# Kernel tuning notes

Hardware: AMD Instinct MI355X
Metric: run time of the kernel (lower is better)

## Reference

```python
import jax, jax.numpy as jnp
import numpy as np

DIM = 512
HEADS = 8
DIM_HEAD = 64
INNER = HEADS * DIM_HEAD  # 512
HIDDEN = 512 * 4          # mlp_dim * expansion
EPS = 1e-5
SCALE = DIM_HEAD ** -0.5


def layernorm(x, w, b):
    mu = jnp.mean(x, axis=-1, keepdims=True)
    var = jnp.var(x, axis=-1, keepdims=True)
    return (x - mu) * jax.lax.rsqrt(var + EPS) * w + b


def setup_inputs() -> dict:
    key = jax.random.key(0)
    ks = jax.random.split(key, 12)
    B, P, N = 2, 8, 1024  # P must equal HEADS (axis-swap bug in original rearrange)
    s = lambda k, shape, fan: jax.random.normal(k, shape, jnp.float32) * (fan ** -0.5)
    return {
        "x": jax.random.normal(ks[0], (B, P, N, DIM), jnp.float32),
        "ln0_w": jnp.ones((DIM,), jnp.float32),
        "ln0_b": jnp.zeros((DIM,), jnp.float32),
        "ln1_w": jnp.ones((DIM,), jnp.float32),
        "ln1_b": jnp.zeros((DIM,), jnp.float32),
        "w_qkv": s(ks[1], (DIM, 3 * INNER), DIM),
        "w_o": s(ks[2], (INNER, DIM), INNER),
        "b_o": jnp.zeros((DIM,), jnp.float32),
        "w1": s(ks[3], (DIM, HIDDEN), DIM),
        "b1": jnp.zeros((HIDDEN,), jnp.float32),
        "w2": s(ks[4], (HIDDEN, DIM), HIDDEN),
        "b2": jnp.zeros((DIM,), jnp.float32),
    }


def reference(x, ln0_w, ln0_b, ln1_w, ln1_b, w_qkv, w_o, b_o, w1, b1, w2, b2):
    B, P, N, _ = x.shape
    x = layernorm(x, ln0_w, ln0_b)  # outer block norm

    # ---- VisionAttention ----
    h = layernorm(x, ln1_w, ln1_b)
    qkv = h @ w_qkv                                    # [B,P,N,3*INNER]
    q, k, v = jnp.split(qkv, 3, axis=-1)
    def to_heads(t):  # [B,P,N,H*D] -> [B,H,P,N,D]
        return t.reshape(B, P, N, HEADS, DIM_HEAD).transpose(0, 3, 1, 2, 4)
    q, k, v = to_heads(q), to_heads(k), to_heads(v)
    dots = jnp.einsum("bhpnd,bhpmd->bhpnm", q, k) * SCALE  # full NxN scores
    attn = jax.nn.softmax(dots, axis=-1)
    out = jnp.einsum("bhpnm,bhpmd->bhpnd", attn, v)        # [B,H,P,N,D]
    # Faithful to buggy rearrange 'b p h n d -> b p n (h d)': swaps H and P axes.
    out = out.transpose(0, 1, 3, 2, 4).reshape(B, HEADS, N, P * DIM_HEAD)
    out = out @ w_o + b_o                                  # [B,H,N,DIM]
    x = out + x  # residual (valid because P == HEADS)

    # ---- MLP ----
    m = jax.nn.gelu(x @ w1 + b1, approximate=False) @ w2 + b2
    return m + x
```

## Files before the change

### kernel.cpp

```cpp
#include <hip/hip_runtime.h>
#include <hip/hip_bf16.h>
#include <math.h>

#define DIMV 512
#define NTOK 16384
#define NSEQ 1024
#define HEADSV 8
#define PPV 8
#define DHEAD 64
#define QKVW 1536
#define HIDV 2048
#define SC2 0.18033688011112042f

typedef unsigned short ushort;
typedef __attribute__((ext_vector_type(8))) short short8;
typedef __attribute__((ext_vector_type(8))) unsigned short ushort8;
typedef __attribute__((ext_vector_type(4))) unsigned short ushortx4;
typedef __attribute__((ext_vector_type(4))) float floatx4;

__device__ __forceinline__ float bf2f(ushort u){
  union { unsigned int i; float f; } c; c.i = ((unsigned int)u) << 16; return c.f;
}
__device__ __forceinline__ ushort f2bf(float f){
  union { float f; unsigned int i; } c; c.f = f;
  unsigned int u = c.i + 0x7fffu + ((c.i >> 16) & 1u);
  return (ushort)(u >> 16);
}
__device__ __forceinline__ ushort f2bf_t(float f){
  union { float f; unsigned int i; } c; c.f = f;
  return (ushort)(c.i >> 16);
}
__device__ __forceinline__ void async_copy16(const void* gptr, void* lptr){
  __builtin_amdgcn_global_load_lds((const __attribute__((address_space(1))) void*)gptr,
                                   (__attribute__((address_space(3))) void*)lptr, 16, 0, 0);
}
__device__ __forceinline__ float fast_gelu(float x){
  float u = x * (2.3022084f + 0.1029435f * x * x);
  return x * __builtin_amdgcn_rcpf(1.f + exp2f(-u));
}

__device__ __forceinline__ void wave_reduce2(float& a, float& b){
  #pragma unroll
  for (int off = 32; off > 0; off >>= 1){
    a += __shfl_down(a, off, 64);
    b += __shfl_down(b, off, 64);
  }
}

__device__ __forceinline__ void wtrans_body(const float* __restrict__ W,
    __hip_bfloat16* __restrict__ Wt, int K, int N, int bx, int by, int t,
    float* tile ){
  int bn = bx * 32, bk = by * 32;
  int tx = t & 31, ty = t >> 5;
  #pragma unroll
  for (int i = 0; i < 32; i += 8)
    tile[(ty + i) * 33 + tx] = W[(size_t)(bk + ty + i) * N + bn + tx];
  __syncthreads();
  #pragma unroll
  for (int i = 0; i < 32; i += 8)
    Wt[(size_t)(bn + ty + i) * K + bk + tx] = __float2bfloat16(tile[tx * 33 + ty + i]);
}

__global__ __launch_bounds__(256) void prep_kernel(const float* __restrict__ x,
    const float* __restrict__ w0, const float* __restrict__ b0,
    const float* __restrict__ w1ln, const float* __restrict__ b1ln,
    __hip_bfloat16* __restrict__ x1, __hip_bfloat16* __restrict__ h,
    const float* __restrict__ wqkv, __hip_bfloat16* __restrict__ wqkvT,
    const float* __restrict__ wo,   __hip_bfloat16* __restrict__ woT,
    const float* __restrict__ w1,   __hip_bfloat16* __restrict__ w1T,
    const float* __restrict__ w2,   __hip_bfloat16* __restrict__ w2T){
  __shared__ float smem[32 * 33];
  int bid = blockIdx.x;
  int t = threadIdx.x;
  if (bid >= NTOK){
    int r = bid - NTOK;
    if (r < 768)        wtrans_body(wqkv, wqkvT, 512, 1536, r % 48, r / 48, t, smem);
    else if (r < 1024){ r -= 768;  wtrans_body(wo, woT, 512, 512,  r % 16, r / 16, t, smem); }
    else if (r < 2048){ r -= 1024; wtrans_body(w1, w1T, 512, 2048, r % 64, r / 64, t, smem); }
    else             { r -= 2048; wtrans_body(w2, w2T, 2048, 512, r % 16, r / 16, t, smem); }
    return;
  }
  float* sm = smem;
  size_t row = bid;
  const float2* xr = (const float2*)(x + row * DIMV);
  float2 v = xr[t];
  float s = v.x + v.y;
  float sq = v.x * v.x + v.y * v.y;
  wave_reduce2(s, sq);
  int wid = t >> 6, lane = t & 63;
  if (lane == 0){ sm[wid] = s; sm[8 + wid] = sq; }
  __syncthreads();
  s  = sm[0] + sm[1] + sm[2] + sm[3];
  sq = sm[8] + sm[9] + sm[10] + sm[11];
  float mu = s * (1.f / DIMV);
  float var = sq * (1.f / DIMV) - mu * mu;
  float r = rsqrtf(var + 1e-5f);
  float2 ww = ((const float2*)w0)[t];
  float2 bb = ((const float2*)b0)[t];
  float2 y;
  y.x = (v.x - mu) * r * ww.x + bb.x;
  y.y = (v.y - mu) * r * ww.y + bb.y;
  ushort2 xb; xb.x = f2bf(y.x); xb.y = f2bf(y.y);
  ((ushort2*)(x1 + row * DIMV))[t] = xb;
  float s2 = y.x + y.y, sq2 = y.x * y.x + y.y * y.y;
  wave_reduce2(s2, sq2);
  __syncthreads();
  if (lane == 0){ sm[wid] = s2; sm[8 + wid] = sq2; }
  __syncthreads();
  s2  = sm[0] + sm[1] + sm[2] + sm[3];
  sq2 = sm[8] + sm[9] + sm[10] + sm[11];
  float mu2 = s2 * (1.f / DIMV);
  float var2 = sq2 * (1.f / DIMV) - mu2 * mu2;
  float r2 = rsqrtf(var2 + 1e-5f);
  float2 w1v = ((const float2*)w1ln)[t];
  float2 b1v = ((const float2*)b1ln)[t];
  float hx = (y.x - mu2) * r2 * w1v.x + b1v.x;
  float hy = (y.y - mu2) * r2 * w1v.y + b1v.y;
  ushort2 hb; hb.x = f2bf(hx); hb.y = f2bf(hy);
  ((ushort2*)(h + row * DIMV))[t] = hb;
}

__global__ __launch_bounds__(256) void gemm_mfma(
    const __hip_bfloat16* __restrict__ A,
    const __hip_bfloat16* __restrict__ Bt,
    const float* __restrict__ bias,
    const __hip_bfloat16* __restrict__ Rb,
    float* __restrict__ Cf,
    __hip_bfloat16* __restrict__ Cb,
    ushort* __restrict__ vt,
    int M, int N, int K, int gx, int dogelu)
{
  __shared__ __hip_bfloat16 As[128 * 32];
  __shared__ __hip_bfloat16 Bs[128 * 32];
  int tid = threadIdx.x;
  int w = tid >> 6, l = tid & 63;

  int bid = blockIdx.x;
  int xcd = bid & 7, idx = bid >> 3;
  int xl = idx % gx, yl = idx / gx;
  size_t bm = (size_t)(xcd * 16 + yl) * 128;
  size_t bn = (size_t)xl * 128;
  int wm = (w & 1) * 64, wn = (w >> 1) * 64;

  int srow = w * 16 + (l >> 2);
  int scol = (l & 3) * 8;
  const __hip_bfloat16* Ag0 = A + (bm + srow) * K + scol;
  const __hip_bfloat16* Ag1 = A + (bm + 64 + srow) * K + scol;
  const __hip_bfloat16* Bg0 = Bt + (bn + srow) * K + scol;
  const __hip_bfloat16* Bg1 = Bt + (bn + 64 + srow) * K + scol;
  __hip_bfloat16* lA0 = &As[srow * 32 + scol];
  __hip_bfloat16* lA1 = &As[(64 + srow) * 32 + scol];
  __hip_bfloat16* lB0 = &Bs[srow * 32 + scol];
  __hip_bfloat16* lB1 = &Bs[(64 + srow) * 32 + scol];

  floatx4 acc[4][4] = {};
  int fm = l & 15;
  int quad = l >> 4;
  int fq = quad * 8;

  for (int k0 = 0; k0 < K; k0 += 32){
    async_copy16(Ag0 + k0, lA0);
    async_copy16(Ag1 + k0, lA1);
    async_copy16(Bg0 + k0, lB0);
    async_copy16(Bg1 + k0, lB1);
    __syncthreads();
    short8 af[4], bf[4];
    #pragma unroll
    for (int i = 0; i < 4; i++){
      af[i] = *(const short8*)&As[(wm + i * 16 + fm) * 32 + fq];
      bf[i] = *(const short8*)&Bs[(wn + i * 16 + fm) * 32 + fq];
    }
    #pragma unroll
    for (int mi = 0; mi < 4; mi++)
      #pragma unroll
      for (int ni = 0; ni < 4; ni++)
        acc[mi][ni] = __builtin_amdgcn_mfma_f32_16x16x32_bf16(af[mi], bf[ni], acc[mi][ni], 0, 0, 0);
    __syncthreads();
  }

  int rq = quad * 4;
  if (vt && bn >= 1024){
    int b = (int)(bm >> 13), p = (int)((bm >> 10) & 7);
    int n0 = (int)(bm & 1023) + wm + rq;
    int cbase = (int)bn + wn - 1024;
    #pragma unroll
    for (int ni = 0; ni < 4; ni++){
      int cc = cbase + ni * 16 + fm;
      int hh = cc >> 6, dd = cc & 63;
      ushort* vdst = vt + ((size_t)((b * 8 + hh) * 8 + p)) * 65536 + (size_t)dd * 1024;
      #pragma unroll
      for (int mi = 0; mi < 4; mi++){
        ushortx4 v4;
        v4[0] = f2bf(acc[mi][ni][0]); v4[1] = f2bf(acc[mi][ni][1]);
        v4[2] = f2bf(acc[mi][ni][2]); v4[3] = f2bf(acc[mi][ni][3]);
        *(ushortx4*)(vdst + n0 + mi * 16) = v4;
      }
    }
  } else if (Cb){
    float scl = (vt && bn < 512) ? SC2 : 1.f;
    #pragma unroll
    for (int ni = 0; ni < 4; ni++){
      size_t col = bn + wn + ni * 16 + fm;
      float bv = bias ? bias[col] : 0.f;
      #pragma unroll
      for (int mi = 0; mi < 4; mi++){
        #pragma unroll
        for (int r = 0; r < 4; r++){
          size_t row = bm + wm + mi * 16 + rq + r;
          float v = acc[mi][ni][r];
          if (vt) v *= scl;
          v += bv;
          if (dogelu) v = fast_gelu(v);
          size_t idx2 = row * N + col;
          if (Rb) v += bf2f(((const ushort*)Rb)[idx2]);
          Cb[idx2] = __hip_bfloat16();
          ((ushort*)Cb)[idx2] = f2bf(v);
        }
      }
    }
  } else {
    #pragma unroll
    for (int ni = 0; ni < 4; ni++){
      size_t col = bn + wn + ni * 16 + fm;
      float bv = bias ? bias[col] : 0.f;
      #pragma unroll
      for (int mi = 0; mi < 4; mi++){
        #pragma unroll
        for (int r = 0; r < 4; r++){
          size_t row = bm + wm + mi * 16 + rq + r;
          float v = acc[mi][ni][r] + bv;
          if (dogelu) v = fast_gelu(v);
          size_t idx2 = row * N + col;
          if (Rb) v += bf2f(((const ushort*)Rb)[idx2]);
          Cf[idx2] = v;
        }
      }
    }
  }
}

__global__ __launch_bounds__(256) void attn_mfma(const __hip_bfloat16* __restrict__ qkvp,
                                                 const ushort* __restrict__ vt,
                                                 __hip_bfloat16* __restrict__ outp){
  __shared__ ushort Ks[64 * 64];
  __shared__ ushort Vs[64 * 64];
  __shared__ ushort Ps[4][32 * 72];
  int tid = threadIdx.x;
  int w = tid >> 6, l = tid & 63;
  int r15 = l & 15, quad = l >> 4, fq = quad * 8;
  int slice = blockIdx.x & 127;
  int qc = blockIdx.x >> 7;
  int b = slice >> 6, hh = (slice >> 3) & 7, p = slice & 7;
  const ushort* base = (const ushort*)qkvp + (size_t)(b * PPV + p) * NSEQ * QKVW;
  const ushort* kb = base + 512 + hh * DHEAD;
  const ushort* vb = vt + (size_t)slice * 65536;

  int q0 = qc * 128 + w * 32;
  short8 qf[2][2];
  #pragma unroll
  for (int mi = 0; mi < 2; mi++)
    #pragma unroll
    for (int kk = 0; kk < 2; kk++)
      qf[mi][kk] = *(const short8*)(base + (size_t)(q0 + mi * 16 + r15) * QKVW + hh * DHEAD + kk * 32 + fq);

  floatx4 o[2][4] = {};
  floatx4 lacc[2] = {};
  short8 ones;
  #pragma unroll
  for (int j = 0; j < 8; j++) ones[j] = (short)0x3F80;

  int s0 = w * 64 + l, s1 = 256 + w * 64 + l;
  int row0 = s0 >> 3, row1 = s1 >> 3;
  int gc0 = (s0 & 7) ^ (row0 & 7), gc1 = (s1 & 7) ^ (row1 & 7);
  const ushort* kp0 = kb + (size_t)row0 * QKVW + gc0 * 8;
  const ushort* kp1 = kb + (size_t)row1 * QKVW + gc1 * 8;
  const ushort* vp0 = vb + (size_t)row0 * 1024 + gc0 * 8;
  const ushort* vp1 = vb + (size_t)row1 * 1024 + gc1 * 8;
  ushort* kd0 = &Ks[s0 * 8]; ushort* kd1 = &Ks[s1 * 8];
  ushort* vd0 = &Vs[s0 * 8]; ushort* vd1 = &Vs[s1 * 8];

  int sw = r15 & 7;

  for (int m0 = 0; m0 < NSEQ; m0 += 64){
    async_copy16(kp0 + (size_t)m0 * QKVW, kd0);
    async_copy16(kp1 + (size_t)m0 * QKVW, kd1);
    async_copy16(vp0 + m0, vd0);
    async_copy16(vp1 + m0, vd1);
    __syncthreads();

    floatx4 s[2][4] = {};
    #pragma unroll
    for (int ni = 0; ni < 4; ni++){
      int row = ni * 16 + r15;
      short8 kf0 = *(const short8*)&Ks[row * 64 + (quad ^ sw) * 8];
      short8 kf1 = *(const short8*)&Ks[row * 64 + ((4 + quad) ^ sw) * 8];
      #pragma unroll
      for (int mi = 0; mi < 2; mi++){
        s[mi][ni] = __builtin_amdgcn_mfma_f32_16x16x32_bf16(qf[mi][0], kf0, s[mi][ni], 0, 0, 0);
        s[mi][ni] = __builtin_amdgcn_mfma_f32_16x16x32_bf16(qf[mi][1], kf1, s[mi][ni], 0, 0, 0);
      }
    }

    #pragma unroll
    for (int mi = 0; mi < 2; mi++)
      #pragma unroll
      for (int ni = 0; ni < 4; ni++)
        #pragma unroll
        for (int r = 0; r < 4; r++)
          Ps[w][(mi * 16 + quad * 4 + r) * 72 + ni * 16 + r15] = f2bf_t(exp2f(s[mi][ni][r]));

    short8 pf[2][2];
    #pragma unroll
    for (int mi = 0; mi < 2; mi++)
      #pragma unroll
      for (int kk = 0; kk < 2; kk++)
        pf[mi][kk] = *(const short8*)&Ps[w][(mi * 16 + r15) * 72 + kk * 32 + fq];

    #pragma unroll
    for (int mi = 0; mi < 2; mi++)
      #pragma unroll
      for (int kk = 0; kk < 2; kk++)
        lacc[mi] = __builtin_amdgcn_mfma_f32_16x16x32_bf16(pf[mi][kk], ones, lacc[mi], 0, 0, 0);

    #pragma unroll
    for (int dj = 0; dj < 4; dj++){
      int d = dj * 16 + r15;
      #pragma unroll
      for (int kk = 0; kk < 2; kk++){
        short8 vf = *(const short8*)&Vs[d * 64 + (((kk * 4 + quad)) ^ sw) * 8];
        #pragma unroll
        for (int mi = 0; mi < 2; mi++)
          o[mi][dj] = __builtin_amdgcn_mfma_f32_16x16x32_bf16(pf[mi][kk], vf, o[mi][dj], 0, 0, 0);
      }
    }
    __syncthreads();
  }

  #pragma unroll
  for (int mi = 0; mi < 2; mi++){
    #pragma unroll
    for (int r = 0; r < 4; r++){
      float inv = __builtin_amdgcn_rcpf(lacc[mi][r]);
      size_t n = q0 + mi * 16 + quad * 4 + r;
      ushort* orow = (ushort*)outp + ((size_t)((b * HEADSV + hh) * NSEQ + n)) * DIMV + p * DHEAD;
      #pragma unroll
      for (int dj = 0; dj < 4; dj++)
        orow[dj * 16 + r15] = f2bf(o[mi][dj][r] * inv);
    }
  }
}

extern "C" void kernel_launch(void* const* d_in, const int* in_sizes, int n_in,
                              void* d_out, int out_size, void* d_ws, size_t ws_size,
                              hipStream_t stream){
  (void)in_sizes; (void)n_in; (void)out_size; (void)ws_size;
  const float* x    = (const float*)d_in[0];
  const float* lw0  = (const float*)d_in[1];
  const float* lb0  = (const float*)d_in[2];
  const float* lw1  = (const float*)d_in[3];
  const float* lb1  = (const float*)d_in[4];
  const float* wqkv = (const float*)d_in[5];
  const float* wo   = (const float*)d_in[6];
  const float* bo   = (const float*)d_in[7];
  const float* w1   = (const float*)d_in[8];
  const float* b1   = (const float*)d_in[9];
  const float* w2   = (const float*)d_in[10];
  const float* b2   = (const float*)d_in[11];
  float* out = (float*)d_out;
  char* ws = (char*)d_ws;
  const size_t MB = 1024 * 1024;

  __hip_bfloat16* x1b  = (__hip_bfloat16*)(ws);
  ushort* vtbuf        = (ushort*)(ws + 32 * MB);
  __hip_bfloat16* x2b  = (__hip_bfloat16*)(ws + 64 * MB);
  __hip_bfloat16* wqkvT= (__hip_bfloat16*)(ws + 80 * MB);
  __hip_bfloat16* woT  = (__hip_bfloat16*)(ws + 82 * MB);
  __hip_bfloat16* w1T  = (__hip_bfloat16*)(ws + 83 * MB);
  __hip_bfloat16* w2T  = (__hip_bfloat16*)(ws + 85 * MB);
  __hip_bfloat16* hB   = (__hip_bfloat16*)(ws + 88 * MB);
  __hip_bfloat16* attnB= hB;
  __hip_bfloat16* qkvB = (__hip_bfloat16*)(ws + 104 * MB);
  __hip_bfloat16* tB   = (__hip_bfloat16*)(ws + 88 * MB);

  prep_kernel<<<NTOK + 3072, 256, 0, stream>>>(
      x, lw0, lb0, lw1, lb1, x1b, hB,
      wqkv, wqkvT, wo, woT, w1, w1T, w2, w2T);

  gemm_mfma<<<(QKVW / 128) * 128, 256, 0, stream>>>(
      hB, wqkvT, nullptr, nullptr, nullptr, qkvB, vtbuf,
      NTOK, QKVW, DIMV, QKVW / 128, 0);

  attn_mfma<<<1024, 256, 0, stream>>>(qkvB, vtbuf, attnB);

  gemm_mfma<<<(DIMV / 128) * 128, 256, 0, stream>>>(
      attnB, woT, bo, x1b, nullptr, x2b, nullptr,
      NTOK, DIMV, DIMV, DIMV / 128, 0);

  gemm_mfma<<<(HIDV / 128) * 128, 256, 0, stream>>>(
      x2b, w1T, b1, nullptr, nullptr, tB, nullptr,
      NTOK, HIDV, DIMV, HIDV / 128, 1);

  gemm_mfma<<<(DIMV / 128) * 128, 256, 0, stream>>>(
      tB, w2T, b2, x2b, out, nullptr, nullptr,
      NTOK, DIMV, HIDV, DIMV / 128, 0);
}
```

Before: 418.5 us.

## Double-buffer LDS tiles in GEMM and attention, swap MFMA operands for vectorized stores

Both the GEMM and attention kernels now double-buffer their shared-memory tiles. The next K/V or A/B tile is prefetched asynchronously while the current one is computed, with explicit vmcnt waits and barriers replacing the full __syncthreads pairs. The MFMA operand order is swapped in the non-QKV GEMMs and in the attention PV and row-sum products, so each lane holds four contiguous output columns. That allows 4-wide vectorized bias loads, residual loads and output stores instead of scalar strided writes. Doubling the LDS footprint may lower occupancy, and the hand-written waitcnt counts must match the number of async copies.

```diff
diff --git a/kernel.cpp b/kernel.cpp
--- a/kernel.cpp
+++ b/kernel.cpp
@@ -120,6 +120,7 @@
   ((ushort2*)(h + row * DIMV))[t] = hb;
 }
 
+template<int SWAP>
 __global__ __launch_bounds__(256) void gemm_mfma(
     const __hip_bfloat16* __restrict__ A,
     const __hip_bfloat16* __restrict__ Bt,
@@ -130,8 +131,8 @@
     ushort* __restrict__ vt,
     int M, int N, int K, int gx, int dogelu)
 {
-  __shared__ __hip_bfloat16 As[128 * 32];
-  __shared__ __hip_bfloat16 Bs[128 * 32];
+  __shared__ __hip_bfloat16 As[2][128 * 32];
+  __shared__ __hip_bfloat16 Bs[2][128 * 32];
   int tid = threadIdx.x;
   int w = tid >> 6, l = tid & 63;
 
@@ -148,91 +149,141 @@
   const __hip_bfloat16* Ag1 = A + (bm + 64 + srow) * K + scol;
   const __hip_bfloat16* Bg0 = Bt + (bn + srow) * K + scol;
   const __hip_bfloat16* Bg1 = Bt + (bn + 64 + srow) * K + scol;
-  __hip_bfloat16* lA0 = &As[srow * 32 + scol];
-  __hip_bfloat16* lA1 = &As[(64 + srow) * 32 + scol];
-  __hip_bfloat16* lB0 = &Bs[srow * 32 + scol];
-  __hip_bfloat16* lB1 = &Bs[(64 + srow) * 32 + scol];
+  int lo = srow * 32 + scol;
 
   floatx4 acc[4][4] = {};
   int fm = l & 15;
   int quad = l >> 4;
   int fq = quad * 8;
 
-  for (int k0 = 0; k0 < K; k0 += 32){
-    async_copy16(Ag0 + k0, lA0);
-    async_copy16(Ag1 + k0, lA1);
-    async_copy16(Bg0 + k0, lB0);
-    async_copy16(Bg1 + k0, lB1);
-    __syncthreads();
+  async_copy16(Ag0, &As[0][lo]);
+  async_copy16(Ag1, &As[0][lo + 64 * 32]);
+  async_copy16(Bg0, &Bs[0][lo]);
+  async_copy16(Bg1, &Bs[0][lo + 64 * 32]);
+
+  int nk = K >> 5;
+  for (int it = 0; it < nk; ++it){
+    int cur = it & 1;
+    if (it + 1 < nk){
+      int nxt = cur ^ 1;
+      int k0 = (it + 1) << 5;
+      async_copy16(Ag0 + k0, &As[nxt][lo]);
+      async_copy16(Ag1 + k0, &As[nxt][lo + 64 * 32]);
+      async_copy16(Bg0 + k0, &Bs[nxt][lo]);
+      async_copy16(Bg1 + k0, &Bs[nxt][lo + 64 * 32]);
+      asm volatile("s_waitcnt vmcnt(4)\n\ts_barrier" ::: "memory");
+    } else {
+      asm volatile("s_waitcnt vmcnt(0)\n\ts_barrier" ::: "memory");
+    }
+    const __hip_bfloat16* Ab = As[cur];
+    const __hip_bfloat16* Bb = Bs[cur];
     short8 af[4], bf[4];
     #pragma unroll
     for (int i = 0; i < 4; i++){
-      af[i] = *(const short8*)&As[(wm + i * 16 + fm) * 32 + fq];
-      bf[i] = *(const short8*)&Bs[(wn + i * 16 + fm) * 32 + fq];
+      af[i] = *(const short8*)&Ab[(wm + i * 16 + fm) * 32 + fq];
+      bf[i] = *(const short8*)&Bb[(wn + i * 16 + fm) * 32 + fq];
     }
     #pragma unroll
     for (int mi = 0; mi < 4; mi++)
       #pragma unroll
-      for (int ni = 0; ni < 4; ni++)
-        acc[mi][ni] = __builtin_amdgcn_mfma_f32_16x16x32_bf16(af[mi], bf[ni], acc[mi][ni], 0, 0, 0);
-    __syncthreads();
+      for (int ni = 0; ni < 4; ni++){
+        if (SWAP)
+          acc[mi][ni] = __builtin_amdgcn_mfma_f32_16x16x32_bf16(bf[ni], af[mi], acc[mi][ni], 0, 0, 0);
+        else
+          acc[mi][ni] = __builtin_amdgcn_mfma_f32_16x16x32_bf16(af[mi], bf[ni], acc[mi][ni], 0, 0, 0);
+      }
+    asm volatile("s_waitcnt lgkmcnt(0)\n\ts_barrier" ::: "memory");
   }
 
   int rq = quad * 4;
-  if (vt && bn >= 1024){
-    int b = (int)(bm >> 13), p = (int)((bm >> 10) & 7);
-    int n0 = (int)(bm & 1023) + wm + rq;
-    int cbase = (int)bn + wn - 1024;
-    #pragma unroll
-    for (int ni = 0; ni < 4; ni++){
-      int cc = cbase + ni * 16 + fm;
-      int hh = cc >> 6, dd = cc & 63;
-      ushort* vdst = vt + ((size_t)((b * 8 + hh) * 8 + p)) * 65536 + (size_t)dd * 1024;
-      #pragma unroll
-      for (int mi = 0; mi < 4; mi++){
-        ushortx4 v4;
-        v4[0] = f2bf(acc[mi][ni][0]); v4[1] = f2bf(acc[mi][ni][1]);
-        v4[2] = f2bf(acc[mi][ni][2]); v4[3] = f2bf(acc[mi][ni][3]);
-        *(ushortx4*)(vdst + n0 + mi * 16) = v4;
-      }
-    }
-  } else if (Cb){
-    float scl = (vt && bn < 512) ? SC2 : 1.f;
-    #pragma unroll
-    for (int ni = 0; ni < 4; ni++){
-      size_t col = bn + wn + ni * 16 + fm;
-      float bv = bias ? bias[col] : 0.f;
-      #pragma unroll
-      for (int mi = 0; mi < 4; mi++){
+  if (SWAP){
+    #pragma unroll
+    for (int mi = 0; mi < 4; mi++){
+      size_t row = bm + wm + mi * 16 + fm;
+      size_t rbase = row * (size_t)N + bn + wn + rq;
+      #pragma unroll
+      for (int ni = 0; ni < 4; ni++){
+        size_t idx2 = rbase + ni * 16;
+        floatx4 v = acc[mi][ni];
+        if (bias){
+          floatx4 bv = *(const floatx4*)(bias + bn + wn + ni * 16 + rq);
+          #pragma unroll
+          for (int r2 = 0; r2 < 4; r2++) v[r2] += bv[r2];
+        }
+        if (dogelu){
+          #pragma unroll
+          for (int r2 = 0; r2 < 4; r2++) v[r2] = fast_gelu(v[r2]);
+        }
+        if (Rb){
+          ushortx4 rb = *(const ushortx4*)((const ushort*)Rb + idx2);
+          #pragma unroll
+          for (int r2 = 0; r2 < 4; r2++) v[r2] += bf2f(rb[r2]);
+        }
+        if (Cb){
+          ushortx4 ob;
+          #pragma unroll
+          for (int r2 = 0; r2 < 4; r2++) ob[r2] = f2bf(v[r2]);
+          *(ushortx4*)((ushort*)Cb + idx2) = ob;
+        } else {
+          *(floatx4*)(Cf + idx2) = v;
+        }
+      }
+    }
+  } else {
+    if (vt && bn >= 1024){
+      int b = (int)(bm >> 13), p = (int)((bm >> 10) & 7);
+      int n0 = (int)(bm & 1023) + wm + rq;
+      int cbase = (int)bn + wn - 1024;
+      #pragma unroll
+      for (int ni = 0; ni < 4; ni++){
+        int cc = cbase + ni * 16 + fm;
+        int hh = cc >> 6, dd = cc & 63;
+        ushort* vdst = vt + ((size_t)((b * 8 + hh) * 8 + p)) * 65536 + (size_t)dd * 1024;
         #pragma unroll
-        for (int r = 0; r < 4; r++){
-          size_t row = bm + wm + mi * 16 + rq + r;
-          float v = acc[mi][ni][r];
-          if (vt) v *= scl;
-          v += bv;
-          if (dogelu) v = fast_gelu(v);
-          size_t idx2 = row * N + col;
-          if (Rb) v += bf2f(((const ushort*)Rb)[idx2]);
-          Cb[idx2] = __hip_bfloat16();
-          ((ushort*)Cb)[idx2] = f2bf(v);
-        }
-      }
-    }
-  } else {
-    #pragma unroll
-    for (int ni = 0; ni < 4; ni++){
-      size_t col = bn + wn + ni * 16 + fm;
-      float bv = bias ? bias[col] : 0.f;
-      #pragma unroll
-      for (int mi = 0; mi < 4; mi++){
+        for (int mi = 0; mi < 4; mi++){
+          ushortx4 v4;
+          v4[0] = f2bf(acc[mi][ni][0]); v4[1] = f2bf(acc[mi][ni][1]);
+          v4[2] = f2bf(acc[mi][ni][2]); v4[3] = f2bf(acc[mi][ni][3]);
+          *(ushortx4*)(vdst + n0 + mi * 16) = v4;
+        }
+      }
+    } else if (Cb){
+      float scl = (vt && bn < 512) ? SC2 : 1.f;
+      #pragma unroll
+      for (int ni = 0; ni < 4; ni++){
+        size_t col = bn + wn + ni * 16 + fm;
+        float bv = bias ? bias[col] : 0.f;
         #pragma unroll
-        for (int r = 0; r < 4; r++){
-          size_t row = bm + wm + mi * 16 + rq + r;
-          float v = acc[mi][ni][r] + bv;
-          if (dogelu) v = fast_gelu(v);
-          size_t idx2 = row * N + col;
-          if (Rb) v += bf2f(((const ushort*)Rb)[idx2]);
-          Cf[idx2] = v;
+        for (int mi = 0; mi < 4; mi++){
+          #pragma unroll
+          for (int r2 = 0; r2 < 4; r2++){
+            size_t row = bm + wm + mi * 16 + rq + r2;
+            float v = acc[mi][ni][r2];
+            if (vt) v *= scl;
+            v += bv;
+            if (dogelu) v = fast_gelu(v);
+            size_t idx2 = row * N + col;
+            if (Rb) v += bf2f(((const ushort*)Rb)[idx2]);
+            ((ushort*)Cb)[idx2] = f2bf(v);
+          }
+        }
+      }
+    } else {
+      #pragma unroll
+      for (int ni = 0; ni < 4; ni++){
+        size_t col = bn + wn + ni * 16 + fm;
+        float bv = bias ? bias[col] : 0.f;
+        #pragma unroll
+        for (int mi = 0; mi < 4; mi++){
+          #pragma unroll
+          for (int r2 = 0; r2 < 4; r2++){
+            size_t row = bm + wm + mi * 16 + rq + r2;
+            float v = acc[mi][ni][r2] + bv;
+            if (dogelu) v = fast_gelu(v);
+            size_t idx2 = row * N + col;
+            if (Rb) v += bf2f(((const ushort*)Rb)[idx2]);
+            Cf[idx2] = v;
+          }
         }
       }
     }
@@ -242,8 +293,8 @@
 __global__ __launch_bounds__(256) void attn_mfma(const __hip_bfloat16* __restrict__ qkvp,
                                                  const ushort* __restrict__ vt,
                                                  __hip_bfloat16* __restrict__ outp){
-  __shared__ ushort Ks[64 * 64];
-  __shared__ ushort Vs[64 * 64];
+  __shared__ ushort Ks[2][64 * 64];
+  __shared__ ushort Vs[2][64 * 64];
   __shared__ ushort Ps[4][32 * 72];
   int tid = threadIdx.x;
   int w = tid >> 6, l = tid & 63;
@@ -255,20 +306,6 @@
   const ushort* kb = base + 512 + hh * DHEAD;
   const ushort* vb = vt + (size_t)slice * 65536;
 
-  int q0 = qc * 128 + w * 32;
-  short8 qf[2][2];
-  #pragma unroll
-  for (int mi = 0; mi < 2; mi++)
-    #pragma unroll
-    for (int kk = 0; kk < 2; kk++)
-      qf[mi][kk] = *(const short8*)(base + (size_t)(q0 + mi * 16 + r15) * QKVW + hh * DHEAD + kk * 32 + fq);
-
-  floatx4 o[2][4] = {};
-  floatx4 lacc[2] = {};
-  short8 ones;
-  #pragma unroll
-  for (int j = 0; j < 8; j++) ones[j] = (short)0x3F80;
-
   int s0 = w * 64 + l, s1 = 256 + w * 64 + l;
   int row0 = s0 >> 3, row1 = s1 >> 3;
   int gc0 = (s0 & 7) ^ (row0 & 7), gc1 = (s1 & 7) ^ (row1 & 7);
@@ -276,24 +313,50 @@
   const ushort* kp1 = kb + (size_t)row1 * QKVW + gc1 * 8;
   const ushort* vp0 = vb + (size_t)row0 * 1024 + gc0 * 8;
   const ushort* vp1 = vb + (size_t)row1 * 1024 + gc1 * 8;
-  ushort* kd0 = &Ks[s0 * 8]; ushort* kd1 = &Ks[s1 * 8];
-  ushort* vd0 = &Vs[s0 * 8]; ushort* vd1 = &Vs[s1 * 8];
+
+  async_copy16(kp0, &Ks[0][s0 * 8]);
+  async_copy16(kp1, &Ks[0][s1 * 8]);
+  async_copy16(vp0, &Vs[0][s0 * 8]);
+  async_copy16(vp1, &Vs[0][s1 * 8]);
+
+  int q0 = qc * 128 + w * 32;
+  short8 qf[2][2];
+  #pragma unroll
+  for (int mi = 0; mi < 2; mi++)
+    #pragma unroll
+    for (int kk = 0; kk < 2; kk++)
+      qf[mi][kk] = *(const short8*)(base + (size_t)(q0 + mi * 16 + r15) * QKVW + hh * DHEAD + kk * 32 + fq);
+
+  floatx4 o[2][4] = {};
+  floatx4 lacc[2] = {};
+  short8 ones;
+  #pragma unroll
+  for (int j = 0; j < 8; j++) ones[j] = (short)0x3F80;
 
   int sw = r15 & 7;
 
-  for (int m0 = 0; m0 < NSEQ; m0 += 64){
-    async_copy16(kp0 + (size_t)m0 * QKVW, kd0);
-    async_copy16(kp1 + (size_t)m0 * QKVW, kd1);
-    async_copy16(vp0 + m0, vd0);
-    async_copy16(vp1 + m0, vd1);
-    __syncthreads();
+  for (int it = 0; it < NSEQ / 64; ++it){
+    int cur = it & 1;
+    if (it + 1 < NSEQ / 64){
+      int nxt = cur ^ 1;
+      size_t m0 = (size_t)(it + 1) * 64;
+      async_copy16(kp0 + m0 * QKVW, &Ks[nxt][s0 * 8]);
+      async_copy16(kp1 + m0 * QKVW, &Ks[nxt][s1 * 8]);
+      async_copy16(vp0 + m0, &Vs[nxt][s0 * 8]);
+      async_copy16(vp1 + m0, &Vs[nxt][s1 * 8]);
+      asm volatile("s_waitcnt vmcnt(4)\n\ts_barrier" ::: "memory");
+    } else {
+      asm volatile("s_waitcnt vmcnt(0)\n\ts_barrier" ::: "memory");
+    }
+    const ushort* Kb = Ks[cur];
+    const ushort* Vb = Vs[cur];
 
     floatx4 s[2][4] = {};
     #pragma unroll
     for (int ni = 0; ni < 4; ni++){
       int row = ni * 16 + r15;
-      short8 kf0 = *(const short8*)&Ks[row * 64 + (quad ^ sw) * 8];
-      short8 kf1 = *(const short8*)&Ks[row * 64 + ((4 + quad) ^ sw) * 8];
+      short8 kf0 = *(const short8*)&Kb[row * 64 + (quad ^ sw) * 8];
+      short8 kf1 = *(const short8*)&Kb[row * 64 + ((4 + quad) ^ sw) * 8];
       #pragma unroll
       for (int mi = 0; mi < 2; mi++){
         s[mi][ni] = __builtin_amdgcn_mfma_f32_16x16x32_bf16(qf[mi][0], kf0, s[mi][ni], 0, 0, 0);
@@ -320,32 +383,33 @@
     for (int mi = 0; mi < 2; mi++)
       #pragma unroll
       for (int kk = 0; kk < 2; kk++)
-        lacc[mi] = __builtin_amdgcn_mfma_f32_16x16x32_bf16(pf[mi][kk], ones, lacc[mi], 0, 0, 0);
+        lacc[mi] = __builtin_amdgcn_mfma_f32_16x16x32_bf16(ones, pf[mi][kk], lacc[mi], 0, 0, 0);
 
     #pragma unroll
     for (int dj = 0; dj < 4; dj++){
       int d = dj * 16 + r15;
       #pragma unroll
       for (int kk = 0; kk < 2; kk++){
-        short8 vf = *(const short8*)&Vs[d * 64 + (((kk * 4 + quad)) ^ sw) * 8];
+        short8 vf = *(const short8*)&Vb[d * 64 + (((kk * 4 + quad)) ^ sw) * 8];
         #pragma unroll
         for (int mi = 0; mi < 2; mi++)
-          o[mi][dj] = __builtin_amdgcn_mfma_f32_16x16x32_bf16(pf[mi][kk], vf, o[mi][dj], 0, 0, 0);
-      }
-    }
-    __syncthreads();
+          o[mi][dj] = __builtin_amdgcn_mfma_f32_16x16x32_bf16(vf, pf[mi][kk], o[mi][dj], 0, 0, 0);
+      }
+    }
+    asm volatile("s_waitcnt lgkmcnt(0)\n\ts_barrier" ::: "memory");
   }
 
   #pragma unroll
   for (int mi = 0; mi < 2; mi++){
-    #pragma unroll
-    for (int r = 0; r < 4; r++){
-      float inv = __builtin_amdgcn_rcpf(lacc[mi][r]);
-      size_t n = q0 + mi * 16 + quad * 4 + r;
-      ushort* orow = (ushort*)outp + ((size_t)((b * HEADSV + hh) * NSEQ + n)) * DIMV + p * DHEAD;
-      #pragma unroll
-      for (int dj = 0; dj < 4; dj++)
-        orow[dj * 16 + r15] = f2bf(o[mi][dj][r] * inv);
+    float inv = __builtin_amdgcn_rcpf(lacc[mi][0]);
+    size_t n = q0 + mi * 16 + r15;
+    ushort* orow = (ushort*)outp + ((size_t)((b * HEADSV + hh) * NSEQ + n)) * DIMV + p * DHEAD + quad * 4;
+    #pragma unroll
+    for (int dj = 0; dj < 4; dj++){
+      ushortx4 ov;
+      #pragma unroll
+      for (int r = 0; r < 4; r++) ov[r] = f2bf(o[mi][dj][r] * inv);
+      *(ushortx4*)(orow + dj * 16) = ov;
     }
   }
 }
@@ -386,21 +450,21 @@
       x, lw0, lb0, lw1, lb1, x1b, hB,
       wqkv, wqkvT, wo, woT, w1, w1T, w2, w2T);
 
-  gemm_mfma<<<(QKVW / 128) * 128, 256, 0, stream>>>(
+  gemm_mfma<0><<<(QKVW / 128) * 128, 256, 0, stream>>>(
       hB, wqkvT, nullptr, nullptr, nullptr, qkvB, vtbuf,
       NTOK, QKVW, DIMV, QKVW / 128, 0);
 
   attn_mfma<<<1024, 256, 0, stream>>>(qkvB, vtbuf, attnB);
 
-  gemm_mfma<<<(DIMV / 128) * 128, 256, 0, stream>>>(
+  gemm_mfma<1><<<(DIMV / 128) * 128, 256, 0, stream>>>(
       attnB, woT, bo, x1b, nullptr, x2b, nullptr,
       NTOK, DIMV, DIMV, DIMV / 128, 0);
 
-  gemm_mfma<<<(HIDV / 128) * 128, 256, 0, stream>>>(
+  gemm_mfma<1><<<(HIDV / 128) * 128, 256, 0, stream>>>(
       x2b, w1T, b1, nullptr, nullptr, tB, nullptr,
       NTOK, HIDV, DIMV, HIDV / 128, 1);
 
-  gemm_mfma<<<(DIMV / 128) * 128, 256, 0, stream>>>(
+  gemm_mfma<1><<<(DIMV / 128) * 128, 256, 0, stream>>>(
       tB, w2T, b2, x2b, out, nullptr, nullptr,
       NTOK, DIMV, HIDV, DIMV / 128, 0);
 }
```

New measurement: 378.9 us. 9.5% less time.
